# Kernel tuning notes

Measured on AMD Instinct MI355X. Metric: run time of the kernel, lower is better.

The kernel has to match this reference:

```python
import jax, jax.numpy as jnp
import numpy as np

D = 896      # mm_hidden_size
H = 8        # num heads
HD = D // H  # head dim = 112
M = 8        # num_memory_tokens
P = 196      # patch_size
EPS = 1e-12


def _layernorm(x, g, b):
    mu = jnp.mean(x, axis=-1, keepdims=True)
    var = jnp.mean(jnp.square(x - mu), axis=-1, keepdims=True)
    return (x - mu) * jax.lax.rsqrt(var + EPS) * g + b


def setup_inputs() -> dict:
    key = jax.random.key(0)
    ks = jax.random.split(key, 12)
    F = 32
    s = 0.02
    return {
        "image_features": jax.random.normal(ks[0], (F, P, D), jnp.float32),
        "initial_memory": jax.random.normal(ks[1], (M, P, D), jnp.float32),
        "qW": jax.random.normal(ks[2], (D, D), jnp.float32) * s,
        "qb": jnp.zeros((D,), jnp.float32),
        "kW": jax.random.normal(ks[3], (D, D), jnp.float32) * s,
        "kb": jnp.zeros((D,), jnp.float32),
        "vW": jax.random.normal(ks[4], (D, D), jnp.float32) * s,
        "vb": jnp.zeros((D,), jnp.float32),
        "oW": jax.random.normal(ks[5], (D, D), jnp.float32) * s,
        "ob": jnp.zeros((D,), jnp.float32),
        "ln1_g": jnp.ones((D,), jnp.float32),
        "ln1_b": jnp.zeros((D,), jnp.float32),
        "mW": jax.random.normal(ks[6], (D, 4 * D), jnp.float32) * s,
        "mb": jnp.zeros((4 * D,), jnp.float32),
        "pW": jax.random.normal(ks[7], (4 * D, D), jnp.float32) * s,
        "pb": jnp.zeros((D,), jnp.float32),
        "ln2_g": jnp.ones((D,), jnp.float32),
        "ln2_b": jnp.zeros((D,), jnp.float32),
    }


def reference(image_features, initial_memory, qW, qb, kW, kb, vW, vb,
              oW, ob, ln1_g, ln1_b, mW, mb, pW, pb, ln2_g, ln2_b):
    F = image_features.shape[0]
    Lq = M * P            # 1568 query tokens
    Lk = F * P            # kv tokens
    mem = initial_memory.reshape(1, Lq, D)      # [1, Lq, D]
    img = image_features.reshape(1, Lk, D)      # [1, Lk, D]

    def heads(x, L):
        return x.reshape(1, L, H, HD).transpose(0, 2, 1, 3)  # [1,H,L,hd]

    q = heads(mem @ qW + qb, Lq)
    k = heads(img @ kW + kb, Lk)
    v = heads(img @ vW + vb, Lk)

    scores = jnp.einsum('bhqd,bhkd->bhqk', q, k) / np.sqrt(HD).astype(jnp.float32)
    probs = jax.nn.softmax(scores, axis=-1)                  # [1,H,Lq,Lk]
    ctx = jnp.einsum('bhqk,bhkd->bhqd', probs, v)
    ctx = ctx.transpose(0, 2, 1, 3).reshape(1, Lq, D)

    # residual + layernorm epilogue of Attention
    attn_out = _layernorm(ctx @ oW + ob + mem, ln1_g, ln1_b)

    # MLP -> residual + layernorm
    hidden = jax.nn.relu(attn_out @ mW + mb)                 # [1, Lq, 4D]
    out = _layernorm(hidden @ pW + pb + attn_out, ln2_g, ln2_b)

    # frame attention scores: sum over heads and query tokens, avg per frame
    attn_sum = probs.sum(axis=(1, 2))[0]                     # [Lk]
    frame_scores = attn_sum.reshape(F, P).mean(axis=1)       # [F]

    final_memory = out.reshape(M, P, D)
    return final_memory, frame_scores
```

## Files before the change

kernel.cpp:

```cpp
#include <hip/hip_runtime.h>
#include <hip/hip_bf16.h>
#include <math.h>

#define TP_D   896
#define TP_H   8
#define TP_HD  112
#define TP_LQ  1568
#define TP_LK  6272
#define TP_D4  3584
#define TP_F   32
#define TP_P   196

typedef unsigned short u16;
typedef float f32x4 __attribute__((ext_vector_type(4)));
typedef __bf16 bf16x8 __attribute__((ext_vector_type(8)));

__device__ inline float bf2f(u16 u) {
    return __uint_as_float(((unsigned int)u) << 16);
}
__device__ inline u16 f2bf(float f) {
    unsigned int x = __float_as_uint(f);
    unsigned int lsb = (x >> 16) & 1u;
    x += 0x7fffu + lsb;
    return (u16)(x >> 16);
}
__device__ inline ushort4 pack4(float a, float b, float c, float d) {
    return make_ushort4(f2bf(a), f2bf(b), f2bf(c), f2bf(d));
}
__device__ inline int pidx(int row, int col) {
    return row * 128 + (col ^ ((row & 7) << 3));
}

__global__ void cast_f32_bf16(const float* __restrict__ src, u16* __restrict__ dst, int n) {
    int i = (blockIdx.x * blockDim.x + threadIdx.x) * 4;
    if (i + 3 < n) {
        float4 v = *(const float4*)(src + i);
        *(ushort4*)(dst + i) = pack4(v.x, v.y, v.z, v.w);
    } else {
        for (; i < n; ++i) dst[i] = f2bf(src[i]);
    }
}

__global__ void cast_div_bf16(const float* __restrict__ src, const float* __restrict__ l,
                              u16* __restrict__ dst) {
    int i = (blockIdx.x * 256 + threadIdx.x) * 4;
    if (i >= TP_LQ * TP_D) return;
    int q = i / TP_D;
    int col = i - q * TP_D;
    int h = col / TP_HD;
    float inv = 1.f / l[h * TP_LQ + q];
    float4 v = *(const float4*)(src + i);
    *(ushort4*)(dst + i) = pack4(v.x * inv, v.y * inv, v.z * inv, v.w * inv);
}

__global__ void transpose_cast(const float* __restrict__ src, u16* __restrict__ dst, int R, int C) {
    __shared__ float t[32][33];
    int bx = blockIdx.x * 32;
    int by = blockIdx.y * 32;
    int tx = threadIdx.x, ty = threadIdx.y;
#pragma unroll
    for (int j = 0; j < 4; ++j)
        t[ty + j * 8][tx] = src[(size_t)(by + ty + j * 8) * C + bx + tx];
    __syncthreads();
#pragma unroll
    for (int j = 0; j < 4; ++j)
        dst[(size_t)(bx + ty + j * 8) * R + by + tx] = f2bf(t[tx][ty + j * 8]);
}

struct GemmParams {
    const u16* A;  long long aZ; int lda;
    const u16* Bt; long long bZ; int ldb;
    int M, N, K;
    const float* bias;
    float* outF;
    u16* outB; long long cZ; int ldc;
    float scale;
    int hbase;
    int relu;
    int kc;
};

#define LDS_STRIDE 56

template <int MODE>
__global__ __launch_bounds__(256, 2) void gemm_bf16(GemmParams p) {
    __shared__ u16 lsA[128 * LDS_STRIDE];
    __shared__ u16 lsB[128 * LDS_STRIDE];

    const int tid = threadIdx.x;
    const int z = blockIdx.z;
    const u16* A;
    const u16* Bt;
    if (MODE == 6) {
        A  = p.A  + (size_t)z * p.kc;
        Bt = p.Bt + (size_t)z * p.kc;
    } else {
        A  = p.A  + (size_t)z * p.aZ;
        Bt = p.Bt + (size_t)z * p.bZ;
    }
    const int m0 = blockIdx.y * 128;
    const int n0 = blockIdx.x * 128;

    const int lane = tid & 63;
    const int w = tid >> 6;
    const int wm = (w >> 1) * 64, wn = (w & 1) * 64;
    const int c = lane & 15, q = lane >> 4;

    f32x4 acc[4][4];
#pragma unroll
    for (int i = 0; i < 4; ++i)
#pragma unroll
        for (int j = 0; j < 4; ++j) acc[i][j] = 0.f;

    const int r0 = tid >> 2;
    const int c8 = (tid & 3) * 8;
    int arow0 = m0 + r0;      if (arow0 >= p.M) arow0 = p.M - 1;
    int arow1 = m0 + r0 + 64; if (arow1 >= p.M) arow1 = p.M - 1;
    int brow0 = n0 + r0;      if (brow0 >= p.N) brow0 = p.N - 1;
    int brow1 = n0 + r0 + 64; if (brow1 >= p.N) brow1 = p.N - 1;
    const u16* a0 = A  + (size_t)arow0 * p.lda + c8;
    const u16* a1 = A  + (size_t)arow1 * p.lda + c8;
    const u16* b0 = Bt + (size_t)brow0 * p.ldb + c8;
    const u16* b1 = Bt + (size_t)brow1 * p.ldb + c8;

    const int KT = (p.K + 31) >> 5;
    for (int kt = 0; kt < KT; ++kt) {
        const int k0 = kt << 5;
        const bool valid = (k0 + c8 + 8) <= p.K;
        uint4 zv = make_uint4(0, 0, 0, 0);
        uint4 va0 = valid ? *(const uint4*)(a0 + k0) : zv;
        uint4 va1 = valid ? *(const uint4*)(a1 + k0) : zv;
        uint4 vb0 = valid ? *(const uint4*)(b0 + k0) : zv;
        uint4 vb1 = valid ? *(const uint4*)(b1 + k0) : zv;
        *(uint4*)(&lsA[r0 * LDS_STRIDE + c8])        = va0;
        *(uint4*)(&lsA[(r0 + 64) * LDS_STRIDE + c8]) = va1;
        *(uint4*)(&lsB[r0 * LDS_STRIDE + c8])        = vb0;
        *(uint4*)(&lsB[(r0 + 64) * LDS_STRIDE + c8]) = vb1;
        __syncthreads();

        bf16x8 af[4], bfv[4];
#pragma unroll
        for (int mi = 0; mi < 4; ++mi)
            af[mi] = *(const bf16x8*)(&lsA[(wm + mi * 16 + c) * LDS_STRIDE + q * 8]);
#pragma unroll
        for (int ni = 0; ni < 4; ++ni)
            bfv[ni] = *(const bf16x8*)(&lsB[(wn + ni * 16 + c) * LDS_STRIDE + q * 8]);
#pragma unroll
        for (int mi = 0; mi < 4; ++mi)
#pragma unroll
            for (int ni = 0; ni < 4; ++ni)
                acc[mi][ni] = __builtin_amdgcn_mfma_f32_16x16x32_bf16(af[mi], bfv[ni], acc[mi][ni], 0, 0, 0);
        __syncthreads();
    }

    if (MODE == 7) {
#pragma unroll
        for (int ni = 0; ni < 4; ++ni) {
            const int col = n0 + wn + ni * 16 + c;
            const float bv = p.bias[col];
#pragma unroll
            for (int mi = 0; mi < 4; ++mi) {
                const int mbase = m0 + wm + mi * 16 + q * 4;
                f32x4 a = acc[mi][ni];
                *(ushort4*)(p.outB + (size_t)col * p.ldc + mbase) =
                    pack4(a[0] + bv, a[1] + bv, a[2] + bv, a[3] + bv);
            }
        }
        return;
    }

#pragma unroll
    for (int mi = 0; mi < 4; ++mi) {
#pragma unroll
        for (int r = 0; r < 4; ++r) {
            const int row = m0 + wm + mi * 16 + q * 4 + r;
            if (row >= p.M) continue;
#pragma unroll
            for (int ni = 0; ni < 4; ++ni) {
                const int col = n0 + wn + ni * 16 + c;
                float v = acc[mi][ni][r];
                if (MODE == 4) {
                    v += p.bias[col];
                    if (p.relu) v = v > 0.f ? v : 0.f;
                    p.outB[(size_t)row * p.ldc + col] = f2bf(v);
                } else if (MODE == 6) {
                    atomicAdd(&p.outF[(size_t)row * p.ldc + col], v);
                }
            }
        }
    }
}

__global__ __launch_bounds__(256, 2) void attn_fused(
        const u16* __restrict__ Qf, const u16* __restrict__ Kf,
        const u16* __restrict__ Vtf, u16* __restrict__ E,
        float* __restrict__ lsum, float* __restrict__ ctxF, float scale) {
    __shared__ u16 lsQ[128 * 128];
    __shared__ u16 lsB[128 * 40];
    __shared__ u16 lsP[128 * 128];

    const int ks  = blockIdx.x;
    const int m0  = blockIdx.y * 128;
    const int h   = blockIdx.z;
    const int tid = threadIdx.x;
    const int lane = tid & 63, w = tid >> 6;
    const int wm = (w >> 1) * 64, wn = (w & 1) * 64;
    const int c = lane & 15, q = lane >> 4;

    {
        const int row = tid >> 1;
        const int half = (tid & 1) * 64;
        int qrow = m0 + row; if (qrow > TP_LQ - 1) qrow = TP_LQ - 1;
        const u16* src = Qf + (size_t)qrow * TP_D + h * TP_HD;
#pragma unroll
        for (int j = 0; j < 8; ++j) {
            int col = half + j * 8;
            uint4 v = make_uint4(0, 0, 0, 0);
            if (col + 8 <= TP_HD) v = *(const uint4*)(src + col);
            *(uint4*)(&lsQ[pidx(row, col)]) = v;
        }
    }

    const int r0 = tid >> 2;
    const int c8 = (tid & 3) * 8;
    const int keybase = ks * 896;

    f32x4 acc_pv[4][4];
#pragma unroll
    for (int i = 0; i < 4; ++i)
#pragma unroll
        for (int j = 0; j < 4; ++j) acc_pv[i][j] = 0.f;
    float rs[4] = {0.f, 0.f, 0.f, 0.f};

    for (int kb = 0; kb < 7; ++kb) {
        const int kblk = keybase + kb * 128;
        f32x4 acc_s[4][4];
#pragma unroll
        for (int i = 0; i < 4; ++i)
#pragma unroll
            for (int j = 0; j < 4; ++j) acc_s[i][j] = 0.f;

#pragma unroll
        for (int kt = 0; kt < 4; ++kt) {
            const int k0 = kt * 32;
            const bool valid = (k0 + c8 + 8) <= TP_HD;
            uint4 zv = make_uint4(0, 0, 0, 0);
            uint4 vb0 = valid ? *(const uint4*)(Kf + (size_t)(kblk + r0) * TP_D + h * TP_HD + k0 + c8) : zv;
            uint4 vb1 = valid ? *(const uint4*)(Kf + (size_t)(kblk + r0 + 64) * TP_D + h * TP_HD + k0 + c8) : zv;
            __syncthreads();
            *(uint4*)(&lsB[r0 * 40 + c8])        = vb0;
            *(uint4*)(&lsB[(r0 + 64) * 40 + c8]) = vb1;
            __syncthreads();
            bf16x8 af[4], bfv[4];
#pragma unroll
            for (int mi = 0; mi < 4; ++mi)
                af[mi] = *(const bf16x8*)(&lsQ[pidx(wm + mi * 16 + c, k0 + q * 8)]);
#pragma unroll
            for (int ni = 0; ni < 4; ++ni)
                bfv[ni] = *(const bf16x8*)(&lsB[(wn + ni * 16 + c) * 40 + q * 8]);
#pragma unroll
            for (int mi = 0; mi < 4; ++mi)
#pragma unroll
                for (int ni = 0; ni < 4; ++ni)
                    acc_s[mi][ni] = __builtin_amdgcn_mfma_f32_16x16x32_bf16(bfv[ni], af[mi], acc_s[mi][ni], 0, 0, 0);
        }

        __syncthreads();
#pragma unroll
        for (int mi = 0; mi < 4; ++mi) {
            const int prow = wm + mi * 16 + c;
            const int qr = m0 + prow;
            const bool qv = qr < TP_LQ;
            float rp = 0.f;
#pragma unroll
            for (int ni = 0; ni < 4; ++ni) {
                float e0, e1, e2, e3;
                {
                    f32x4 a = acc_s[mi][ni];
                    e0 = __expf(fminf(a[0] * scale, 30.f));
                    e1 = __expf(fminf(a[1] * scale, 30.f));
                    e2 = __expf(fminf(a[2] * scale, 30.f));
                    e3 = __expf(fminf(a[3] * scale, 30.f));
                }
                rp += (e0 + e1) + (e2 + e3);
                ushort4 pk = pack4(e0, e1, e2, e3);
                const int kcol = wn + ni * 16 + q * 4;
                if (qv)
                    *(ushort4*)(E + ((size_t)h * TP_LQ + qr) * TP_LK + kblk + kcol) = pk;
                *(ushort4*)(&lsP[pidx(prow, kcol)]) = pk;
            }
            rs[mi] += rp;
        }

#pragma unroll
        for (int kt = 0; kt < 4; ++kt) {
            const int kk = kblk + kt * 32 + c8;
            int d0 = r0;
            int d1 = r0 + 64; if (d1 > TP_HD - 1) d1 = TP_HD - 1;
            uint4 vb0 = *(const uint4*)(Vtf + ((size_t)h * TP_HD + d0) * TP_LK + kk);
            uint4 vb1 = *(const uint4*)(Vtf + ((size_t)h * TP_HD + d1) * TP_LK + kk);
            __syncthreads();
            *(uint4*)(&lsB[r0 * 40 + c8])        = vb0;
            *(uint4*)(&lsB[(r0 + 64) * 40 + c8]) = vb1;
            __syncthreads();
            bf16x8 ap[4], bv[4];
#pragma unroll
            for (int mi = 0; mi < 4; ++mi)
                ap[mi] = *(const bf16x8*)(&lsP[pidx(wm + mi * 16 + c, kt * 32 + q * 8)]);
#pragma unroll
            for (int ni = 0; ni < 4; ++ni)
                bv[ni] = *(const bf16x8*)(&lsB[(wn + ni * 16 + c) * 40 + q * 8]);
#pragma unroll
            for (int mi = 0; mi < 4; ++mi)
#pragma unroll
                for (int ni = 0; ni < 4; ++ni)
                    acc_pv[mi][ni] = __builtin_amdgcn_mfma_f32_16x16x32_bf16(ap[mi], bv[ni], acc_pv[mi][ni], 0, 0, 0);
        }
    }

#pragma unroll
    for (int mi = 0; mi < 4; ++mi) {
        float rp = rs[mi];
        rp += __shfl_xor(rp, 16, 64);
        rp += __shfl_xor(rp, 32, 64);
        const int qr = m0 + wm + mi * 16 + c;
        if (q == 0 && qr < TP_LQ) atomicAdd(&lsum[h * TP_LQ + qr], rp);
    }
#pragma unroll
    for (int mi = 0; mi < 4; ++mi) {
#pragma unroll
        for (int r = 0; r < 4; ++r) {
            const int qr = m0 + wm + mi * 16 + q * 4 + r;
            if (qr >= TP_LQ) continue;
#pragma unroll
            for (int ni = 0; ni < 4; ++ni) {
                const int d = wn + ni * 16 + c;
                if (d < TP_HD)
                    atomicAdd(&ctxF[(size_t)qr * TP_D + h * TP_HD + d], acc_pv[mi][ni][r]);
            }
        }
    }
}

__global__ void colsum_kernel(const u16* __restrict__ E, const float* __restrict__ l,
                              float* __restrict__ colsum, int nrows) {
    int c4 = blockIdx.x * 256 + threadIdx.x;
    if (c4 >= TP_LK / 4) return;
    int chunk = (nrows + gridDim.y - 1) / gridDim.y;
    int r0 = blockIdx.y * chunk;
    int r1 = r0 + chunk; if (r1 > nrows) r1 = nrows;
    float a0 = 0.f, a1 = 0.f, a2 = 0.f, a3 = 0.f;
    for (int r = r0; r < r1; ++r) {
        float inv = 1.f / l[r];
        ushort4 u = ((const ushort4*)(E + (size_t)r * TP_LK))[c4];
        a0 += bf2f(u.x) * inv; a1 += bf2f(u.y) * inv;
        a2 += bf2f(u.z) * inv; a3 += bf2f(u.w) * inv;
    }
    atomicAdd(&colsum[4 * c4 + 0], a0);
    atomicAdd(&colsum[4 * c4 + 1], a1);
    atomicAdd(&colsum[4 * c4 + 2], a2);
    atomicAdd(&colsum[4 * c4 + 3], a3);
}

__global__ __launch_bounds__(256) void layernorm_rows(const float* __restrict__ x,
        const float* __restrict__ bias, const float* __restrict__ res,
        const float* __restrict__ g, const float* __restrict__ b,
        float* __restrict__ outF, u16* __restrict__ outB) {
    const int tid = threadIdx.x;
    const float* xr = x + (size_t)blockIdx.x * TP_D;
    const float* rr = res + (size_t)blockIdx.x * TP_D;
    float v[4];
#pragma unroll
    for (int i = 0; i < 4; ++i) {
        int idx = tid + i * 256;
        v[i] = (idx < TP_D) ? (xr[idx] + bias[idx] + rr[idx]) : 0.f;
    }
    float s = v[0] + v[1] + v[2] + v[3];
    __shared__ float red[4];
#pragma unroll
    for (int o = 32; o > 0; o >>= 1) s += __shfl_xor(s, o, 64);
    if ((tid & 63) == 0) red[tid >> 6] = s;
    __syncthreads();
    const float mu = (red[0] + red[1] + red[2] + red[3]) * (1.f / TP_D);
    __syncthreads();
    float ss = 0.f;
#pragma unroll
    for (int i = 0; i < 4; ++i) {
        int idx = tid + i * 256;
        if (idx < TP_D) { float d = v[i] - mu; ss += d * d; }
    }
#pragma unroll
    for (int o = 32; o > 0; o >>= 1) ss += __shfl_xor(ss, o, 64);
    if ((tid & 63) == 0) red[tid >> 6] = ss;
    __syncthreads();
    const float var = (red[0] + red[1] + red[2] + red[3]) * (1.f / TP_D);
    const float rs = rsqrtf(var + 1e-12f);
    float* of = outF + (size_t)blockIdx.x * TP_D;
    u16* obp = outB ? outB + (size_t)blockIdx.x * TP_D : nullptr;
#pragma unroll
    for (int i = 0; i < 4; ++i) {
        int idx = tid + i * 256;
        if (idx < TP_D) {
            float y = (v[i] - mu) * rs * g[idx] + b[idx];
            of[idx] = y;
            if (obp) obp[idx] = f2bf(y);
        }
    }
}

__global__ void frame_scores_kernel(const float* __restrict__ colsum, float* __restrict__ out) {
    const int tid = threadIdx.x;
    float v = (tid < TP_P) ? colsum[blockIdx.x * TP_P + tid] : 0.f;
    __shared__ float red[4];
#pragma unroll
    for (int o = 32; o > 0; o >>= 1) v += __shfl_xor(v, o, 64);
    if ((tid & 63) == 0) red[tid >> 6] = v;
    __syncthreads();
    if (tid == 0) out[blockIdx.x] = (red[0] + red[1] + red[2] + red[3]) * (1.f / TP_P);
}

extern "C" void kernel_launch(void* const* d_in, const int* in_sizes, int n_in,
                              void* d_out, int out_size, void* d_ws, size_t ws_size,
                              hipStream_t stream) {
    const float* img  = (const float*)d_in[0];
    const float* mem  = (const float*)d_in[1];
    const float* qW   = (const float*)d_in[2];
    const float* qb   = (const float*)d_in[3];
    const float* kW   = (const float*)d_in[4];
    const float* kb   = (const float*)d_in[5];
    const float* vW   = (const float*)d_in[6];
    const float* vb   = (const float*)d_in[7];
    const float* oW   = (const float*)d_in[8];
    const float* ob   = (const float*)d_in[9];
    const float* ln1g = (const float*)d_in[10];
    const float* ln1b = (const float*)d_in[11];
    const float* mW   = (const float*)d_in[12];
    const float* mb   = (const float*)d_in[13];
    const float* pW   = (const float*)d_in[14];
    const float* pb   = (const float*)d_in[15];
    const float* ln2g = (const float*)d_in[16];
    const float* ln2b = (const float*)d_in[17];
    float* out = (float*)d_out;

    char* base = (char*)d_ws;
    size_t off = 0;
    auto take = [&](size_t nbytes) -> void* {
        void* p = base + off;
        off += (nbytes + 255) & ~(size_t)255;
        return p;
    };

    u16* imgB  = (u16*)take((size_t)TP_LK * TP_D * 2);
    u16* memB  = (u16*)take((size_t)TP_LQ * TP_D * 2);
    u16* qWt   = (u16*)take((size_t)TP_D * TP_D * 2);
    u16* kWt   = (u16*)take((size_t)TP_D * TP_D * 2);
    u16* vWt   = (u16*)take((size_t)TP_D * TP_D * 2);
    u16* oWt   = (u16*)take((size_t)TP_D * TP_D * 2);
    u16* mWt   = (u16*)take((size_t)TP_D * TP_D4 * 2);
    u16* pWt   = (u16*)take((size_t)TP_D * TP_D4 * 2);
    u16* Qf    = (u16*)take((size_t)TP_LQ * TP_D * 2);
    u16* Kf    = (u16*)take((size_t)TP_LK * TP_D * 2);
    u16* Vtf   = (u16*)take((size_t)TP_LK * TP_D * 2);
    float* ctxF  = (float*)take((size_t)TP_LQ * TP_D * 4);
    u16* ctxB  = (u16*)take((size_t)TP_LQ * TP_D * 2);
    float* pre1  = (float*)take((size_t)TP_LQ * TP_D * 4);
    float* attn  = (float*)take((size_t)TP_LQ * TP_D * 4);
    u16* attnB = (u16*)take((size_t)TP_LQ * TP_D * 2);
    u16* hidden= (u16*)take((size_t)TP_LQ * TP_D4 * 2);
    float* pre2  = (float*)take((size_t)TP_LQ * TP_D * 4);
    float* colsum= (float*)take((size_t)TP_LK * 4);
    float* lsum  = (float*)take((size_t)TP_H * TP_LQ * 4);
    u16* E     = (u16*)take((size_t)TP_H * TP_LQ * TP_LK * 2);

    cast_f32_bf16<<<(TP_LK * TP_D / 4 + 255) / 256, 256, 0, stream>>>(img, imgB, TP_LK * TP_D);
    cast_f32_bf16<<<(TP_LQ * TP_D / 4 + 255) / 256, 256, 0, stream>>>(mem, memB, TP_LQ * TP_D);
    transpose_cast<<<dim3(28, 28), dim3(32, 8), 0, stream>>>(qW, qWt, TP_D, TP_D);
    transpose_cast<<<dim3(28, 28), dim3(32, 8), 0, stream>>>(kW, kWt, TP_D, TP_D);
    transpose_cast<<<dim3(28, 28), dim3(32, 8), 0, stream>>>(vW, vWt, TP_D, TP_D);
    transpose_cast<<<dim3(28, 28), dim3(32, 8), 0, stream>>>(oW, oWt, TP_D, TP_D);
    transpose_cast<<<dim3(TP_D4 / 32, TP_D / 32), dim3(32, 8), 0, stream>>>(mW, mWt, TP_D, TP_D4);
    transpose_cast<<<dim3(TP_D / 32, TP_D4 / 32), dim3(32, 8), 0, stream>>>(pW, pWt, TP_D4, TP_D);
    hipMemsetAsync(colsum, 0, (size_t)TP_LK * 4, stream);
    hipMemsetAsync(lsum, 0, (size_t)TP_H * TP_LQ * 4, stream);
    hipMemsetAsync(ctxF, 0, (size_t)TP_LQ * TP_D * 4, stream);
    hipMemsetAsync(pre1, 0, (size_t)TP_LQ * TP_D * 4, stream);
    hipMemsetAsync(pre2, 0, (size_t)TP_LQ * TP_D * 4, stream);

    {
        GemmParams p{};
        p.A = memB; p.aZ = 0; p.lda = TP_D;
        p.Bt = qWt; p.bZ = 0; p.ldb = TP_D;
        p.M = TP_LQ; p.N = TP_D; p.K = TP_D;
        p.bias = qb; p.outB = Qf; p.ldc = TP_D; p.relu = 0;
        gemm_bf16<4><<<dim3(7, 13, 1), 256, 0, stream>>>(p);
    }
    {
        GemmParams p{};
        p.A = imgB; p.aZ = 0; p.lda = TP_D;
        p.Bt = kWt; p.bZ = 0; p.ldb = TP_D;
        p.M = TP_LK; p.N = TP_D; p.K = TP_D;
        p.bias = kb; p.outB = Kf; p.ldc = TP_D; p.relu = 0;
        gemm_bf16<4><<<dim3(7, 49, 1), 256, 0, stream>>>(p);
    }
    {
        GemmParams p{};
        p.A = imgB; p.aZ = 0; p.lda = TP_D;
        p.Bt = vWt; p.bZ = 0; p.ldb = TP_D;
        p.M = TP_LK; p.N = TP_D; p.K = TP_D;
        p.bias = vb; p.outB = Vtf; p.ldc = TP_LK;
        gemm_bf16<7><<<dim3(7, 49, 1), 256, 0, stream>>>(p);
    }

    const float scale = 0.09449111825230679f;
    attn_fused<<<dim3(7, 13, TP_H), 256, 0, stream>>>(Qf, Kf, Vtf, E, lsum, ctxF, scale);
    colsum_kernel<<<dim3(7, 224), 256, 0, stream>>>(E, lsum, colsum, TP_H * TP_LQ);
    cast_div_bf16<<<(TP_LQ * TP_D / 4 + 255) / 256, 256, 0, stream>>>(ctxF, lsum, ctxB);

    {
        GemmParams p{};
        p.A = ctxB; p.lda = TP_D;
        p.Bt = oWt; p.ldb = TP_D;
        p.M = TP_LQ; p.N = TP_D; p.K = 448; p.kc = 448;
        p.outF = pre1; p.ldc = TP_D;
        gemm_bf16<6><<<dim3(7, 13, 2), 256, 0, stream>>>(p);
    }
    layernorm_rows<<<TP_LQ, 256, 0, stream>>>(pre1, ob, mem, ln1g, ln1b, attn, attnB);

    {
        GemmParams p{};
        p.A = attnB; p.aZ = 0; p.lda = TP_D;
        p.Bt = mWt; p.bZ = 0; p.ldb = TP_D;
        p.M = TP_LQ; p.N = TP_D4; p.K = TP_D;
        p.bias = mb; p.outB = hidden; p.ldc = TP_D4; p.relu = 1;
        gemm_bf16<4><<<dim3(28, 13, 1), 256, 0, stream>>>(p);
    }
    {
        GemmParams p{};
        p.A = hidden; p.lda = TP_D4;
        p.Bt = pWt; p.ldb = TP_D4;
        p.M = TP_LQ; p.N = TP_D; p.K = 896; p.kc = 896;
        p.outF = pre2; p.ldc = TP_D;
        gemm_bf16<6><<<dim3(7, 13, 4), 256, 0, stream>>>(p);
    }
    layernorm_rows<<<TP_LQ, 256, 0, stream>>>(pre2, pb, attn, ln2g, ln2b, out, nullptr);

    frame_scores_kernel<<<TP_F, 256, 0, stream>>>(colsum, out + (size_t)TP_LQ * TP_D);
}
```

Measured before the change: 557.9 us.

## Split attention into two passes, recompute scores instead of materializing E

Removes the huge bf16 E matrix (H*Lq*Lk) write and the separate colsum pass. A first kernel computes the softmax row sums, and a second recomputes QK^T, normalizes, accumulates column sums via shuffles and atomics, and does PV. The key loads are double-buffered and the query tiles shrink to 64 rows. Separately, the GEMMs switch to 128x64 tiles with higher occupancy, and the memsets are merged into one. This trades doubled QK^T compute and more atomics for avoiding roughly 150MB of global traffic.

```diff
diff --git a/kernel.cpp b/kernel.cpp
--- a/kernel.cpp
+++ b/kernel.cpp
@@ -68,49 +68,44 @@
 }
 
 struct GemmParams {
-    const u16* A;  long long aZ; int lda;
-    const u16* Bt; long long bZ; int ldb;
+    const u16* A;  int lda;
+    const u16* Bt; int ldb;
     int M, N, K;
     const float* bias;
     float* outF;
-    u16* outB; long long cZ; int ldc;
-    float scale;
-    int hbase;
+    u16* outB; int ldc;
     int relu;
     int kc;
 };
 
 #define LDS_STRIDE 56
 
-template <int MODE>
-__global__ __launch_bounds__(256, 2) void gemm_bf16(GemmParams p) {
+template <int MODE, int NT>
+__global__ __launch_bounds__(256, 4) void gemm_bf16(GemmParams p) {
     __shared__ u16 lsA[128 * LDS_STRIDE];
-    __shared__ u16 lsB[128 * LDS_STRIDE];
+    __shared__ u16 lsB[NT * 32 * LDS_STRIDE];
 
     const int tid = threadIdx.x;
     const int z = blockIdx.z;
-    const u16* A;
-    const u16* Bt;
+    const u16* A  = p.A;
+    const u16* Bt = p.Bt;
     if (MODE == 6) {
-        A  = p.A  + (size_t)z * p.kc;
-        Bt = p.Bt + (size_t)z * p.kc;
-    } else {
-        A  = p.A  + (size_t)z * p.aZ;
-        Bt = p.Bt + (size_t)z * p.bZ;
+        A  += (size_t)z * p.kc;
+        Bt += (size_t)z * p.kc;
     }
     const int m0 = blockIdx.y * 128;
-    const int n0 = blockIdx.x * 128;
+    const int n0 = blockIdx.x * (NT * 32);
 
     const int lane = tid & 63;
     const int w = tid >> 6;
-    const int wm = (w >> 1) * 64, wn = (w & 1) * 64;
+    const int wm = (w >> 1) * 64, wn = (w & 1) * (16 * NT);
     const int c = lane & 15, q = lane >> 4;
 
-    f32x4 acc[4][4];
+    f32x4 acc[4][NT];
 #pragma unroll
     for (int i = 0; i < 4; ++i)
 #pragma unroll
-        for (int j = 0; j < 4; ++j) acc[i][j] = 0.f;
+        for (int j = 0; j < NT; ++j) acc[i][j] = 0.f;
 
     const int r0 = tid >> 2;
     const int c8 = (tid & 3) * 8;
@@ -131,31 +126,32 @@
         uint4 va0 = valid ? *(const uint4*)(a0 + k0) : zv;
         uint4 va1 = valid ? *(const uint4*)(a1 + k0) : zv;
         uint4 vb0 = valid ? *(const uint4*)(b0 + k0) : zv;
-        uint4 vb1 = valid ? *(const uint4*)(b1 + k0) : zv;
+        uint4 vb1 = (NT == 4 && valid) ? *(const uint4*)(b1 + k0) : zv;
         *(uint4*)(&lsA[r0 * LDS_STRIDE + c8])        = va0;
         *(uint4*)(&lsA[(r0 + 64) * LDS_STRIDE + c8]) = va1;
         *(uint4*)(&lsB[r0 * LDS_STRIDE + c8])        = vb0;
-        *(uint4*)(&lsB[(r0 + 64) * LDS_STRIDE + c8]) = vb1;
+        if (NT == 4)
+            *(uint4*)(&lsB[(r0 + 64) * LDS_STRIDE + c8]) = vb1;
         __syncthreads();
 
-        bf16x8 af[4], bfv[4];
+        bf16x8 af[4], bfv[NT];
 #pragma unroll
         for (int mi = 0; mi < 4; ++mi)
             af[mi] = *(const bf16x8*)(&lsA[(wm + mi * 16 + c) * LDS_STRIDE + q * 8]);
 #pragma unroll
-        for (int ni = 0; ni < 4; ++ni)
+        for (int ni = 0; ni < NT; ++ni)
             bfv[ni] = *(const bf16x8*)(&lsB[(wn + ni * 16 + c) * LDS_STRIDE + q * 8]);
 #pragma unroll
         for (int mi = 0; mi < 4; ++mi)
 #pragma unroll
-            for (int ni = 0; ni < 4; ++ni)
+            for (int ni = 0; ni < NT; ++ni)
                 acc[mi][ni] = __builtin_amdgcn_mfma_f32_16x16x32_bf16(af[mi], bfv[ni], acc[mi][ni], 0, 0, 0);
         __syncthreads();
     }
 
     if (MODE == 7) {
 #pragma unroll
-        for (int ni = 0; ni < 4; ++ni) {
+        for (int ni = 0; ni < NT; ++ni) {
             const int col = n0 + wn + ni * 16 + c;
             const float bv = p.bias[col];
 #pragma unroll
@@ -176,7 +172,7 @@
             const int row = m0 + wm + mi * 16 + q * 4 + r;
             if (row >= p.M) continue;
 #pragma unroll
-            for (int ni = 0; ni < 4; ++ni) {
+            for (int ni = 0; ni < NT; ++ni) {
                 const int col = n0 + wn + ni * 16 + c;
                 float v = acc[mi][ni][r];
                 if (MODE == 4) {
@@ -191,175 +187,267 @@
     }
 }
 
-__global__ __launch_bounds__(256, 2) void attn_fused(
+__global__ __launch_bounds__(256, 4) void attn_lsum(
         const u16* __restrict__ Qf, const u16* __restrict__ Kf,
-        const u16* __restrict__ Vtf, u16* __restrict__ E,
-        float* __restrict__ lsum, float* __restrict__ ctxF, float scale) {
-    __shared__ u16 lsQ[128 * 128];
-    __shared__ u16 lsB[128 * 40];
-    __shared__ u16 lsP[128 * 128];
-
-    const int ks  = blockIdx.x;
-    const int m0  = blockIdx.y * 128;
-    const int h   = blockIdx.z;
+        float* __restrict__ lsum, float scale) {
+    __shared__ u16 lsQ[64 * 128];
+    __shared__ u16 lsB[2][128 * 40];
+
+    const int ks = blockIdx.x;
+    const int m0 = blockIdx.y * 64;
+    const int h  = blockIdx.z;
     const int tid = threadIdx.x;
     const int lane = tid & 63, w = tid >> 6;
-    const int wm = (w >> 1) * 64, wn = (w & 1) * 64;
+    const int wn = w * 32;
     const int c = lane & 15, q = lane >> 4;
 
     {
-        const int row = tid >> 1;
-        const int half = (tid & 1) * 64;
+        const int row = tid & 63;
+        const int cg  = (tid >> 6) * 32;
         int qrow = m0 + row; if (qrow > TP_LQ - 1) qrow = TP_LQ - 1;
         const u16* src = Qf + (size_t)qrow * TP_D + h * TP_HD;
 #pragma unroll
-        for (int j = 0; j < 8; ++j) {
-            int col = half + j * 8;
+        for (int j = 0; j < 4; ++j) {
+            int col = cg + j * 8;
             uint4 v = make_uint4(0, 0, 0, 0);
             if (col + 8 <= TP_HD) v = *(const uint4*)(src + col);
             *(uint4*)(&lsQ[pidx(row, col)]) = v;
         }
     }
 
-    const int r0 = tid >> 2;
-    const int c8 = (tid & 3) * 8;
+    const int r0 = tid >> 2, c8 = (tid & 3) * 8;
     const int keybase = ks * 896;
-
-    f32x4 acc_pv[4][4];
-#pragma unroll
-    for (int i = 0; i < 4; ++i)
-#pragma unroll
-        for (int j = 0; j < 4; ++j) acc_pv[i][j] = 0.f;
     float rs[4] = {0.f, 0.f, 0.f, 0.f};
 
     for (int kb = 0; kb < 7; ++kb) {
         const int kblk = keybase + kb * 128;
-        f32x4 acc_s[4][4];
-#pragma unroll
-        for (int i = 0; i < 4; ++i)
-#pragma unroll
-            for (int j = 0; j < 4; ++j) acc_s[i][j] = 0.f;
-
+        f32x4 acc[4][2];
+#pragma unroll
+        for (int i = 0; i < 4; ++i) { acc[i][0] = 0.f; acc[i][1] = 0.f; }
+
+        uint4 nv0, nv1;
+        {
+            const uint4 zv = make_uint4(0, 0, 0, 0);
+            bool v = (c8 + 8) <= TP_HD;
+            nv0 = v ? *(const uint4*)(Kf + (size_t)(kblk + r0) * TP_D + h * TP_HD + c8) : zv;
+            nv1 = v ? *(const uint4*)(Kf + (size_t)(kblk + r0 + 64) * TP_D + h * TP_HD + c8) : zv;
+        }
 #pragma unroll
         for (int kt = 0; kt < 4; ++kt) {
-            const int k0 = kt * 32;
-            const bool valid = (k0 + c8 + 8) <= TP_HD;
-            uint4 zv = make_uint4(0, 0, 0, 0);
-            uint4 vb0 = valid ? *(const uint4*)(Kf + (size_t)(kblk + r0) * TP_D + h * TP_HD + k0 + c8) : zv;
-            uint4 vb1 = valid ? *(const uint4*)(Kf + (size_t)(kblk + r0 + 64) * TP_D + h * TP_HD + k0 + c8) : zv;
+            uint4 cv0 = nv0, cv1 = nv1;
+            if (kt < 3) {
+                const uint4 zv = make_uint4(0, 0, 0, 0);
+                const int k0 = (kt + 1) * 32;
+                bool v = (k0 + c8 + 8) <= TP_HD;
+                nv0 = v ? *(const uint4*)(Kf + (size_t)(kblk + r0) * TP_D + h * TP_HD + k0 + c8) : zv;
+                nv1 = v ? *(const uint4*)(Kf + (size_t)(kblk + r0 + 64) * TP_D + h * TP_HD + k0 + c8) : zv;
+            }
+            u16* Bb = lsB[kt & 1];
+            *(uint4*)(&Bb[r0 * 40 + c8])        = cv0;
+            *(uint4*)(&Bb[(r0 + 64) * 40 + c8]) = cv1;
             __syncthreads();
-            *(uint4*)(&lsB[r0 * 40 + c8])        = vb0;
-            *(uint4*)(&lsB[(r0 + 64) * 40 + c8]) = vb1;
-            __syncthreads();
-            bf16x8 af[4], bfv[4];
+            bf16x8 af[4], bfv[2];
 #pragma unroll
             for (int mi = 0; mi < 4; ++mi)
-                af[mi] = *(const bf16x8*)(&lsQ[pidx(wm + mi * 16 + c, k0 + q * 8)]);
-#pragma unroll
-            for (int ni = 0; ni < 4; ++ni)
-                bfv[ni] = *(const bf16x8*)(&lsB[(wn + ni * 16 + c) * 40 + q * 8]);
+                af[mi] = *(const bf16x8*)(&lsQ[pidx(mi * 16 + c, kt * 32 + q * 8)]);
+#pragma unroll
+            for (int ni = 0; ni < 2; ++ni)
+                bfv[ni] = *(const bf16x8*)(&Bb[(wn + ni * 16 + c) * 40 + q * 8]);
 #pragma unroll
             for (int mi = 0; mi < 4; ++mi)
 #pragma unroll
-                for (int ni = 0; ni < 4; ++ni)
-                    acc_s[mi][ni] = __builtin_amdgcn_mfma_f32_16x16x32_bf16(bfv[ni], af[mi], acc_s[mi][ni], 0, 0, 0);
-        }
-
-        __syncthreads();
+                for (int ni = 0; ni < 2; ++ni)
+                    acc[mi][ni] = __builtin_amdgcn_mfma_f32_16x16x32_bf16(bfv[ni], af[mi], acc[mi][ni], 0, 0, 0);
+        }
 #pragma unroll
         for (int mi = 0; mi < 4; ++mi) {
-            const int prow = wm + mi * 16 + c;
-            const int qr = m0 + prow;
-            const bool qv = qr < TP_LQ;
             float rp = 0.f;
 #pragma unroll
-            for (int ni = 0; ni < 4; ++ni) {
-                float e0, e1, e2, e3;
-                {
-                    f32x4 a = acc_s[mi][ni];
-                    e0 = __expf(fminf(a[0] * scale, 30.f));
-                    e1 = __expf(fminf(a[1] * scale, 30.f));
-                    e2 = __expf(fminf(a[2] * scale, 30.f));
-                    e3 = __expf(fminf(a[3] * scale, 30.f));
-                }
-                rp += (e0 + e1) + (e2 + e3);
-                ushort4 pk = pack4(e0, e1, e2, e3);
-                const int kcol = wn + ni * 16 + q * 4;
-                if (qv)
-                    *(ushort4*)(E + ((size_t)h * TP_LQ + qr) * TP_LK + kblk + kcol) = pk;
-                *(ushort4*)(&lsP[pidx(prow, kcol)]) = pk;
+            for (int ni = 0; ni < 2; ++ni) {
+                f32x4 a = acc[mi][ni];
+#pragma unroll
+                for (int r = 0; r < 4; ++r)
+                    rp += __expf(fminf(a[r] * scale, 30.f));
             }
             rs[mi] += rp;
         }
-
-#pragma unroll
-        for (int kt = 0; kt < 4; ++kt) {
-            const int kk = kblk + kt * 32 + c8;
-            int d0 = r0;
-            int d1 = r0 + 64; if (d1 > TP_HD - 1) d1 = TP_HD - 1;
-            uint4 vb0 = *(const uint4*)(Vtf + ((size_t)h * TP_HD + d0) * TP_LK + kk);
-            uint4 vb1 = *(const uint4*)(Vtf + ((size_t)h * TP_HD + d1) * TP_LK + kk);
-            __syncthreads();
-            *(uint4*)(&lsB[r0 * 40 + c8])        = vb0;
-            *(uint4*)(&lsB[(r0 + 64) * 40 + c8]) = vb1;
-            __syncthreads();
-            bf16x8 ap[4], bv[4];
-#pragma unroll
-            for (int mi = 0; mi < 4; ++mi)
-                ap[mi] = *(const bf16x8*)(&lsP[pidx(wm + mi * 16 + c, kt * 32 + q * 8)]);
-#pragma unroll
-            for (int ni = 0; ni < 4; ++ni)
-                bv[ni] = *(const bf16x8*)(&lsB[(wn + ni * 16 + c) * 40 + q * 8]);
-#pragma unroll
-            for (int mi = 0; mi < 4; ++mi)
-#pragma unroll
-                for (int ni = 0; ni < 4; ++ni)
-                    acc_pv[mi][ni] = __builtin_amdgcn_mfma_f32_16x16x32_bf16(ap[mi], bv[ni], acc_pv[mi][ni], 0, 0, 0);
-        }
-    }
-
+    }
 #pragma unroll
     for (int mi = 0; mi < 4; ++mi) {
         float rp = rs[mi];
         rp += __shfl_xor(rp, 16, 64);
         rp += __shfl_xor(rp, 32, 64);
-        const int qr = m0 + wm + mi * 16 + c;
+        const int qr = m0 + mi * 16 + c;
         if (q == 0 && qr < TP_LQ) atomicAdd(&lsum[h * TP_LQ + qr], rp);
     }
+}
+
+__global__ __launch_bounds__(256, 3) void attn_pv(
+        const u16* __restrict__ Qf, const u16* __restrict__ Kf,
+        const u16* __restrict__ Vtf, const float* __restrict__ lsum,
+        float* __restrict__ ctxF, float* __restrict__ colsum, float scale) {
+    __shared__ u16 lsQ[64 * 128];
+    __shared__ u16 lsP[64 * 128];
+    __shared__ u16 lsB[2][128 * 40];
+
+    const int ks = blockIdx.x;
+    const int m0 = blockIdx.y * 64;
+    const int h  = blockIdx.z;
+    const int tid = threadIdx.x;
+    const int lane = tid & 63, w = tid >> 6;
+    const int wn = w * 32;
+    const int c = lane & 15, q = lane >> 4;
+
+    {
+        const int row = tid & 63;
+        const int cg  = (tid >> 6) * 32;
+        int qrow = m0 + row; if (qrow > TP_LQ - 1) qrow = TP_LQ - 1;
+        const u16* src = Qf + (size_t)qrow * TP_D + h * TP_HD;
+#pragma unroll
+        for (int j = 0; j < 4; ++j) {
+            int col = cg + j * 8;
+            uint4 v = make_uint4(0, 0, 0, 0);
+            if (col + 8 <= TP_HD) v = *(const uint4*)(src + col);
+            *(uint4*)(&lsQ[pidx(row, col)]) = v;
+        }
+    }
+
+    float linv[4];
 #pragma unroll
     for (int mi = 0; mi < 4; ++mi) {
+        const int qr = m0 + mi * 16 + c;
+        linv[mi] = (qr < TP_LQ) ? 1.f / lsum[h * TP_LQ + qr] : 0.f;
+    }
+
+    const int r0 = tid >> 2, c8 = (tid & 3) * 8;
+    const int keybase = ks * 896;
+
+    f32x4 apv[4][2];
+#pragma unroll
+    for (int i = 0; i < 4; ++i) { apv[i][0] = 0.f; apv[i][1] = 0.f; }
+
+    for (int kb = 0; kb < 7; ++kb) {
+        const int kblk = keybase + kb * 128;
+        f32x4 acc[4][2];
+#pragma unroll
+        for (int i = 0; i < 4; ++i) { acc[i][0] = 0.f; acc[i][1] = 0.f; }
+
+        uint4 nv0, nv1;
+        {
+            const uint4 zv = make_uint4(0, 0, 0, 0);
+            bool v = (c8 + 8) <= TP_HD;
+            nv0 = v ? *(const uint4*)(Kf + (size_t)(kblk + r0) * TP_D + h * TP_HD + c8) : zv;
+            nv1 = v ? *(const uint4*)(Kf + (size_t)(kblk + r0 + 64) * TP_D + h * TP_HD + c8) : zv;
+        }
+#pragma unroll
+        for (int kt = 0; kt < 4; ++kt) {
+            uint4 cv0 = nv0, cv1 = nv1;
+            if (kt < 3) {
+                const uint4 zv = make_uint4(0, 0, 0, 0);
+                const int k0 = (kt + 1) * 32;
+                bool v = (k0 + c8 + 8) <= TP_HD;
+                nv0 = v ? *(const uint4*)(Kf + (size_t)(kblk + r0) * TP_D + h * TP_HD + k0 + c8) : zv;
+                nv1 = v ? *(const uint4*)(Kf + (size_t)(kblk + r0 + 64) * TP_D + h * TP_HD + k0 + c8) : zv;
+            }
+            u16* Bb = lsB[kt & 1];
+            *(uint4*)(&Bb[r0 * 40 + c8])        = cv0;
+            *(uint4*)(&Bb[(r0 + 64) * 40 + c8]) = cv1;
+            __syncthreads();
+            bf16x8 af[4], bfv[2];
+#pragma unroll
+            for (int mi = 0; mi < 4; ++mi)
+                af[mi] = *(const bf16x8*)(&lsQ[pidx(mi * 16 + c, kt * 32 + q * 8)]);
+#pragma unroll
+            for (int ni = 0; ni < 2; ++ni)
+                bfv[ni] = *(const bf16x8*)(&Bb[(wn + ni * 16 + c) * 40 + q * 8]);
+#pragma unroll
+            for (int mi = 0; mi < 4; ++mi)
+#pragma unroll
+                for (int ni = 0; ni < 2; ++ni)
+                    acc[mi][ni] = __builtin_amdgcn_mfma_f32_16x16x32_bf16(bfv[ni], af[mi], acc[mi][ni], 0, 0, 0);
+        }
+
+        float part[2][4];
+#pragma unroll
+        for (int ni = 0; ni < 2; ++ni)
+#pragma unroll
+            for (int r = 0; r < 4; ++r) part[ni][r] = 0.f;
+#pragma unroll
+        for (int mi = 0; mi < 4; ++mi) {
+            const int prow = mi * 16 + c;
+#pragma unroll
+            for (int ni = 0; ni < 2; ++ni) {
+                f32x4 a = acc[mi][ni];
+                float e0 = __expf(fminf(a[0] * scale, 30.f));
+                float e1 = __expf(fminf(a[1] * scale, 30.f));
+                float e2 = __expf(fminf(a[2] * scale, 30.f));
+                float e3 = __expf(fminf(a[3] * scale, 30.f));
+                *(ushort4*)(&lsP[pidx(prow, wn + ni * 16 + q * 4)]) = pack4(e0, e1, e2, e3);
+                const float li = linv[mi];
+                part[ni][0] += e0 * li; part[ni][1] += e1 * li;
+                part[ni][2] += e2 * li; part[ni][3] += e3 * li;
+            }
+        }
+#pragma unroll
+        for (int ni = 0; ni < 2; ++ni)
+#pragma unroll
+            for (int r = 0; r < 4; ++r) {
+                float v = part[ni][r];
+                v += __shfl_xor(v, 1, 64);
+                v += __shfl_xor(v, 2, 64);
+                v += __shfl_xor(v, 4, 64);
+                v += __shfl_xor(v, 8, 64);
+                if (c == 0) atomicAdd(&colsum[kblk + wn + ni * 16 + q * 4 + r], v);
+            }
+
+        uint4 wv0, wv1;
+        {
+            int d1 = r0 + 64; if (d1 > TP_HD - 1) d1 = TP_HD - 1;
+            wv0 = *(const uint4*)(Vtf + ((size_t)h * TP_HD + r0) * TP_LK + kblk + c8);
+            wv1 = *(const uint4*)(Vtf + ((size_t)h * TP_HD + d1) * TP_LK + kblk + c8);
+        }
+#pragma unroll
+        for (int kt = 0; kt < 4; ++kt) {
+            uint4 cv0 = wv0, cv1 = wv1;
+            if (kt < 3) {
+                const int kk = kblk + (kt + 1) * 32 + c8;
+                int d1 = r0 + 64; if (d1 > TP_HD - 1) d1 = TP_HD - 1;
+                wv0 = *(const uint4*)(Vtf + ((size_t)h * TP_HD + r0) * TP_LK + kk);
+                wv1 = *(const uint4*)(Vtf + ((size_t)h * TP_HD + d1) * TP_LK + kk);
+            }
+            u16* Bb = lsB[kt & 1];
+            *(uint4*)(&Bb[r0 * 40 + c8])        = cv0;
+            *(uint4*)(&Bb[(r0 + 64) * 40 + c8]) = cv1;
+            __syncthreads();
+            bf16x8 ap[4], bv[2];
+#pragma unroll
+            for (int mi = 0; mi < 4; ++mi)
+                ap[mi] = *(const bf16x8*)(&lsP[pidx(mi * 16 + c, kt * 32 + q * 8)]);
+#pragma unroll
+            for (int ni = 0; ni < 2; ++ni)
+                bv[ni] = *(const bf16x8*)(&Bb[(wn + ni * 16 + c) * 40 + q * 8]);
+#pragma unroll
+            for (int mi = 0; mi < 4; ++mi)
+#pragma unroll
+                for (int ni = 0; ni < 2; ++ni)
+                    apv[mi][ni] = __builtin_amdgcn_mfma_f32_16x16x32_bf16(ap[mi], bv[ni], apv[mi][ni], 0, 0, 0);
+        }
+    }
+
+#pragma unroll
+    for (int mi = 0; mi < 4; ++mi) {
 #pragma unroll
         for (int r = 0; r < 4; ++r) {
-            const int qr = m0 + wm + mi * 16 + q * 4 + r;
+            const int qr = m0 + mi * 16 + q * 4 + r;
             if (qr >= TP_LQ) continue;
 #pragma unroll
-            for (int ni = 0; ni < 4; ++ni) {
+            for (int ni = 0; ni < 2; ++ni) {
                 const int d = wn + ni * 16 + c;
                 if (d < TP_HD)
-                    atomicAdd(&ctxF[(size_t)qr * TP_D + h * TP_HD + d], acc_pv[mi][ni][r]);
-            }
-        }
-    }
-}
-
-__global__ void colsum_kernel(const u16* __restrict__ E, const float* __restrict__ l,
-                              float* __restrict__ colsum, int nrows) {
-    int c4 = blockIdx.x * 256 + threadIdx.x;
-    if (c4 >= TP_LK / 4) return;
-    int chunk = (nrows + gridDim.y - 1) / gridDim.y;
-    int r0 = blockIdx.y * chunk;
-    int r1 = r0 + chunk; if (r1 > nrows) r1 = nrows;
-    float a0 = 0.f, a1 = 0.f, a2 = 0.f, a3 = 0.f;
-    for (int r = r0; r < r1; ++r) {
-        float inv = 1.f / l[r];
-        ushort4 u = ((const ushort4*)(E + (size_t)r * TP_LK))[c4];
-        a0 += bf2f(u.x) * inv; a1 += bf2f(u.y) * inv;
-        a2 += bf2f(u.z) * inv; a3 += bf2f(u.w) * inv;
-    }
-    atomicAdd(&colsum[4 * c4 + 0], a0);
-    atomicAdd(&colsum[4 * c4 + 1], a1);
-    atomicAdd(&colsum[4 * c4 + 2], a2);
-    atomicAdd(&colsum[4 * c4 + 3], a3);
+                    atomicAdd(&ctxF[(size_t)qr * TP_D + h * TP_HD + d], apv[mi][ni][r]);
+            }
+        }
+    }
 }
 
 __global__ __launch_bounds__(256) void layernorm_rows(const float* __restrict__ x,
@@ -461,16 +549,16 @@
     u16* Qf    = (u16*)take((size_t)TP_LQ * TP_D * 2);
     u16* Kf    = (u16*)take((size_t)TP_LK * TP_D * 2);
     u16* Vtf   = (u16*)take((size_t)TP_LK * TP_D * 2);
-    float* ctxF  = (float*)take((size_t)TP_LQ * TP_D * 4);
     u16* ctxB  = (u16*)take((size_t)TP_LQ * TP_D * 2);
-    float* pre1  = (float*)take((size_t)TP_LQ * TP_D * 4);
     float* attn  = (float*)take((size_t)TP_LQ * TP_D * 4);
     u16* attnB = (u16*)take((size_t)TP_LQ * TP_D * 2);
     u16* hidden= (u16*)take((size_t)TP_LQ * TP_D4 * 2);
+    float* ctxF  = (float*)take((size_t)TP_LQ * TP_D * 4);
+    float* pre1  = (float*)take((size_t)TP_LQ * TP_D * 4);
     float* pre2  = (float*)take((size_t)TP_LQ * TP_D * 4);
     float* colsum= (float*)take((size_t)TP_LK * 4);
     float* lsum  = (float*)take((size_t)TP_H * TP_LQ * 4);
-    u16* E     = (u16*)take((size_t)TP_H * TP_LQ * TP_LK * 2);
+    size_t zlen = (char*)(lsum + TP_H * TP_LQ) - (char*)ctxF;
 
     cast_f32_bf16<<<(TP_LK * TP_D / 4 + 255) / 256, 256, 0, stream>>>(img, imgB, TP_LK * TP_D);
     cast_f32_bf16<<<(TP_LQ * TP_D / 4 + 255) / 256, 256, 0, stream>>>(mem, memB, TP_LQ * TP_D);
@@ -480,40 +568,36 @@
     transpose_cast<<<dim3(28, 28), dim3(32, 8), 0, stream>>>(oW, oWt, TP_D, TP_D);
     transpose_cast<<<dim3(TP_D4 / 32, TP_D / 32), dim3(32, 8), 0, stream>>>(mW, mWt, TP_D, TP_D4);
     transpose_cast<<<dim3(TP_D / 32, TP_D4 / 32), dim3(32, 8), 0, stream>>>(pW, pWt, TP_D4, TP_D);
-    hipMemsetAsync(colsum, 0, (size_t)TP_LK * 4, stream);
-    hipMemsetAsync(lsum, 0, (size_t)TP_H * TP_LQ * 4, stream);
-    hipMemsetAsync(ctxF, 0, (size_t)TP_LQ * TP_D * 4, stream);
-    hipMemsetAsync(pre1, 0, (size_t)TP_LQ * TP_D * 4, stream);
-    hipMemsetAsync(pre2, 0, (size_t)TP_LQ * TP_D * 4, stream);
+    hipMemsetAsync(ctxF, 0, zlen, stream);
 
     {
         GemmParams p{};
-        p.A = memB; p.aZ = 0; p.lda = TP_D;
-        p.Bt = qWt; p.bZ = 0; p.ldb = TP_D;
+        p.A = memB; p.lda = TP_D;
+        p.Bt = qWt; p.ldb = TP_D;
         p.M = TP_LQ; p.N = TP_D; p.K = TP_D;
         p.bias = qb; p.outB = Qf; p.ldc = TP_D; p.relu = 0;
-        gemm_bf16<4><<<dim3(7, 13, 1), 256, 0, stream>>>(p);
+        gemm_bf16<4, 2><<<dim3(14, 13, 1), 256, 0, stream>>>(p);
     }
     {
         GemmParams p{};
-        p.A = imgB; p.aZ = 0; p.lda = TP_D;
-        p.Bt = kWt; p.bZ = 0; p.ldb = TP_D;
+        p.A = imgB; p.lda = TP_D;
+        p.Bt = kWt; p.ldb = TP_D;
         p.M = TP_LK; p.N = TP_D; p.K = TP_D;
         p.bias = kb; p.outB = Kf; p.ldc = TP_D; p.relu = 0;
-        gemm_bf16<4><<<dim3(7, 49, 1), 256, 0, stream>>>(p);
+        gemm_bf16<4, 2><<<dim3(14, 49, 1), 256, 0, stream>>>(p);
     }
     {
         GemmParams p{};
-        p.A = imgB; p.aZ = 0; p.lda = TP_D;
-        p.Bt = vWt; p.bZ = 0; p.ldb = TP_D;
+        p.A = imgB; p.lda = TP_D;
+        p.Bt = vWt; p.ldb = TP_D;
         p.M = TP_LK; p.N = TP_D; p.K = TP_D;
         p.bias = vb; p.outB = Vtf; p.ldc = TP_LK;
-        gemm_bf16<7><<<dim3(7, 49, 1), 256, 0, stream>>>(p);
+        gemm_bf16<7, 2><<<dim3(14, 49, 1), 256, 0, stream>>>(p);
     }
 
     const float scale = 0.09449111825230679f;
-    attn_fused<<<dim3(7, 13, TP_H), 256, 0, stream>>>(Qf, Kf, Vtf, E, lsum, ctxF, scale);
-    colsum_kernel<<<dim3(7, 224), 256, 0, stream>>>(E, lsum, colsum, TP_H * TP_LQ);
+    attn_lsum<<<dim3(7, 25, TP_H), 256, 0, stream>>>(Qf, Kf, lsum, scale);
+    attn_pv<<<dim3(7, 25, TP_H), 256, 0, stream>>>(Qf, Kf, Vtf, lsum, ctxF, colsum, scale);
     cast_div_bf16<<<(TP_LQ * TP_D / 4 + 255) / 256, 256, 0, stream>>>(ctxF, lsum, ctxB);
 
     {
@@ -522,17 +606,17 @@
         p.Bt = oWt; p.ldb = TP_D;
         p.M = TP_LQ; p.N = TP_D; p.K = 448; p.kc = 448;
         p.outF = pre1; p.ldc = TP_D;
-        gemm_bf16<6><<<dim3(7, 13, 2), 256, 0, stream>>>(p);
+        gemm_bf16<6, 2><<<dim3(14, 13, 2), 256, 0, stream>>>(p);
     }
     layernorm_rows<<<TP_LQ, 256, 0, stream>>>(pre1, ob, mem, ln1g, ln1b, attn, attnB);
 
     {
         GemmParams p{};
-        p.A = attnB; p.aZ = 0; p.lda = TP_D;
-        p.Bt = mWt; p.bZ = 0; p.ldb = TP_D;
+        p.A = attnB; p.lda = TP_D;
+        p.Bt = mWt; p.ldb = TP_D;
         p.M = TP_LQ; p.N = TP_D4; p.K = TP_D;
         p.bias = mb; p.outB = hidden; p.ldc = TP_D4; p.relu = 1;
-        gemm_bf16<4><<<dim3(28, 13, 1), 256, 0, stream>>>(p);
+        gemm_bf16<4, 2><<<dim3(56, 13, 1), 256, 0, stream>>>(p);
     }
     {
         GemmParams p{};
@@ -540,7 +624,7 @@
         p.Bt = pWt; p.ldb = TP_D4;
         p.M = TP_LQ; p.N = TP_D; p.K = 896; p.kc = 896;
         p.outF = pre2; p.ldc = TP_D;
-        gemm_bf16<6><<<dim3(7, 13, 4), 256, 0, stream>>>(p);
+        gemm_bf16<6, 2><<<dim3(14, 13, 4), 256, 0, stream>>>(p);
     }
     layernorm_rows<<<TP_LQ, 256, 0, stream>>>(pre2, pb, attn, ln2g, ln2b, out, nullptr);
 
```

Result: slower. 595.9 us (+6.8%).
